# Optimization experiments

Hardware: AMD Instinct MI355X
Metric: run time of the kernel (lower is better)

The kernel has to match this reference:

```python
import jax, jax.numpy as jnp
import numpy as np

N, E, D = 50000, 800000, 64  # nodes, edges, hidden (in_hid == out_hid, n_heads == 1)


def setup_inputs() -> dict:
    key = jax.random.key(0)
    ks = jax.random.split(key, 12)

    def lin(k, out_d, in_d):
        k1, k2 = jax.random.split(k)
        s = 1.0 / np.sqrt(in_d)
        W = jax.random.uniform(k1, (out_d, in_d), minval=-s, maxval=s, dtype=jnp.float32)
        b = jax.random.uniform(k2, (out_d,), minval=-s, maxval=s, dtype=jnp.float32)
        return W, b

    Wt, bt = lin(ks[0], D, D + 1)   # w_transfer: Linear(d_input+1, d_k)
    Wq, bq = lin(ks[1], D, D)
    Wks, bks = lin(ks[2], D, D)
    Wkd, bkd = lin(ks[3], D, D)
    Wvs, bvs = lin(ks[4], D, D)
    Wvd, bvd = lin(ks[5], D, D)
    return {
        "x": jax.random.normal(ks[6], (N, D), dtype=jnp.float32),
        "edge_index": jax.random.randint(ks[7], (2, E), 0, N),
        "edge_time": jax.random.uniform(ks[8], (E,), dtype=jnp.float32),
        "x_time": jax.random.uniform(ks[9], (N,), dtype=jnp.float32),
        "edge_same": jax.random.randint(ks[10], (E,), 0, 2).astype(jnp.float32),
        "ln_gamma": jnp.ones((D,), jnp.float32),
        "ln_beta": jnp.zeros((D,), jnp.float32),
        "Wt": Wt, "bt": bt, "Wq": Wq, "bq": bq,
        "Wks": Wks, "bks": bks, "Wkd": Wkd, "bkd": bkd,
        "Wvs": Wvs, "bvs": bvs, "Wvd": Wvd, "bvd": bvd,
    }


def _gelu(x):
    return jax.nn.gelu(x, approximate=False)  # torch F.gelu default (erf)


def _temporal_enc(t):
    # TemporalEncoding: div_term[j] = 1/10000^(2*(j//2)/D); sin on even cols, cos on odd
    j = jnp.arange(D)
    div = 1.0 / jnp.power(jnp.float32(10000.0), (2.0 * (j // 2)).astype(jnp.float32) / D)
    pe = (t.reshape(-1, 1) * 200.0) * div[None, :]  # [E, D]
    return jnp.where((j % 2 == 0)[None, :], jnp.sin(pe), jnp.cos(pe))


def reference(x, edge_index, edge_time, x_time, edge_same, ln_gamma, ln_beta,
              Wt, bt, Wq, bq, Wks, bks, Wkd, bkd, Wvs, bvs, Wvd, bvd):
    residual = x
    # LayerNorm(d_input)
    mu = jnp.mean(x, axis=-1, keepdims=True)
    var = jnp.var(x, axis=-1, keepdims=True)
    xn = (x - mu) / jnp.sqrt(var + 1e-5) * ln_gamma + ln_beta

    src, dst = edge_index[0], edge_index[1]  # x_j = source, x_i = target (PyG default)
    x_j = xn[src]                            # [E, D] gather
    x_i = xn[dst]                            # [E, D] gather
    es = edge_same.reshape(-1, 1)            # [E, 1]

    te = _temporal_enc(edge_time)            # [E, D]
    xt = _gelu(jnp.concatenate([x_j, edge_time.reshape(-1, 1)], axis=1) @ Wt.T + bt) + te

    q = x_i @ Wq.T + bq
    k = es * (xt @ Wks.T + bks) + (1.0 - es) * (xt @ Wkd.T + bkd)
    att = jnp.sum(k * q, axis=-1) / jnp.sqrt(jnp.float32(D))  # [E]

    # PyG-style segment softmax over edges sharing the same receiver
    m = jax.ops.segment_max(att, dst, num_segments=N)
    m = jnp.where(jnp.isfinite(m), m, 0.0)
    ex = jnp.exp(att - m[dst])
    denom = jax.ops.segment_sum(ex, dst, num_segments=N)
    attn = ex / (denom[dst] + 1e-16)         # [E]

    v = es * (xt @ Wvs.T + bvs) + (1.0 - es) * (xt @ Wvd.T + bvd)
    aggr = jax.ops.segment_sum(attn[:, None] * v, dst, num_segments=N)  # [N, D]

    return residual + _gelu(aggr)            # dropout is identity in eval
```

## Files before the change

kernel.cpp:

```cpp
#include <hip/hip_runtime.h>
#include <hip/hip_bf16.h>
#include <math.h>

#define D 64

typedef __attribute__((ext_vector_type(8))) short bf16x8;
typedef __attribute__((ext_vector_type(8))) _Float16 f16x8;
typedef __attribute__((ext_vector_type(8))) unsigned short u16x8;
typedef __attribute__((ext_vector_type(4))) float f32x4;
typedef unsigned short u16;

__device__ __forceinline__ float gelu_erf(float x) {
    return 0.5f * x * (1.0f + erff(x * 0.70710678118654752f));
}
__device__ __forceinline__ float gelu_fast(float x) {
    float t = x * fmaf(x * x, -0.1029432f, -2.3022080f);
    float e = __builtin_amdgcn_exp2f(t);
    return x * __builtin_amdgcn_rcpf(1.0f + e);
}
__device__ __forceinline__ u16 f2bf(float v) {
    __hip_bfloat16 h = __float2bfloat16(v);
    return *(u16*)&h;
}
__device__ __forceinline__ float bf2f(u16 v) {
    return __uint_as_float(((unsigned int)v) << 16);
}
__device__ __forceinline__ u16 f2h(float v) {
    _Float16 h = (_Float16)v;
    return __builtin_bit_cast(u16, h);
}
__device__ __forceinline__ void atomic_pk_add_f16(u16* addr, float lo, float hi) {
    unsigned int p = (unsigned int)f2h(lo) | ((unsigned int)f2h(hi) << 16);
    asm volatile("global_atomic_pk_add_f16 %0, %1, off sc1" :: "v"(addr), "v"(p));
}
__device__ __forceinline__ int pi_perm(int p) { return ((p & 3) << 4) | (p >> 2); }

__device__ __forceinline__ float rowsum16(float v) {
    int x;
    x = __builtin_amdgcn_update_dpp(0, __builtin_bit_cast(int, v), 0xB1, 0xF, 0xF, true);
    v += __builtin_bit_cast(float, x);
    x = __builtin_amdgcn_update_dpp(0, __builtin_bit_cast(int, v), 0x4E, 0xF, 0xF, true);
    v += __builtin_bit_cast(float, x);
    x = __builtin_amdgcn_update_dpp(0, __builtin_bit_cast(int, v), 0x141, 0xF, 0xF, true);
    v += __builtin_bit_cast(float, x);
    x = __builtin_amdgcn_update_dpp(0, __builtin_bit_cast(int, v), 0x140, 0xF, 0xF, true);
    v += __builtin_bit_cast(float, x);
    return v;
}

__global__ __launch_bounds__(256) void prep_hist(
    const float* __restrict__ Wt, const float* __restrict__ Wq,
    const float* __restrict__ Wks, const float* __restrict__ Wkd,
    const float* __restrict__ Wvs, const float* __restrict__ Wvd,
    u16* __restrict__ WtB, u16* __restrict__ WqB,
    u16* __restrict__ WksB, u16* __restrict__ WkdB,
    u16* __restrict__ WvsB, u16* __restrict__ WvdB,
    const int* __restrict__ ei, const float* __restrict__ esame,
    int* __restrict__ cnt, int* __restrict__ rank, int E)
{
    if (blockIdx.x < 12) {
        int task = blockIdx.x * 4 + (threadIdx.x >> 6);
        int lane = threadIdx.x & 63;
        int wsel = task >> 3, f = task & 7;
        int c = lane & 15, quad = lane >> 4;
        int nt = f >> 1, kk = f & 1;
        for (int j = 0; j < 8; ++j) {
            int n = nt * 16 + c, k = kk * 32 + quad * 8 + j;
            float v; u16* dp; bool h16 = false;
            switch (wsel) {
                case 0: v = Wt[n * 65 + k];  dp = WtB;  break;
                case 1: v = Wq[n * 64 + k];  dp = WqB;  break;
                case 2: v = Wks[k * 64 + n]; dp = WksB; break;
                case 3: v = Wkd[k * 64 + n]; dp = WkdB; break;
                case 4: v = Wvs[n * 64 + pi_perm(k)]; dp = WvsB; h16 = true; break;
                default: v = Wvd[n * 64 + pi_perm(k)]; dp = WvdB; h16 = true; break;
            }
            dp[(f * 64 + lane) * 8 + j] = h16 ? f2h(v) : f2bf(v);
        }
    } else {
        int gid = (blockIdx.x - 12) * 256 + threadIdx.x;
        int stride = (gridDim.x - 12) * 256;
        int e[4]; bool v[4]; int key[4];
        #pragma unroll
        for (int j = 0; j < 4; ++j) { e[j] = gid + j * stride; v[j] = e[j] < E; }
        #pragma unroll
        for (int j = 0; j < 4; ++j) {
            if (v[j]) key[j] = 2 * ei[E + e[j]] + (esame[e[j]] > 0.5f ? 0 : 1);
        }
        int r[4];
        #pragma unroll
        for (int j = 0; j < 4; ++j) {
            if (v[j]) r[j] = atomicAdd(&cnt[key[j]], 1);
        }
        #pragma unroll
        for (int j = 0; j < 4; ++j) {
            if (v[j]) rank[e[j]] = r[j];
        }
    }
}

#define SCAN_CHUNK 2048

__global__ __launch_bounds__(256) void scan_phaseA(const int* __restrict__ cnt,
                                                   int* __restrict__ bsum, int M)
{
    int base = blockIdx.x * SCAN_CHUNK;
    int s = 0;
    for (int i = threadIdx.x; i < SCAN_CHUNK; i += 256) {
        int idx = base + i;
        s += (idx < M) ? cnt[idx] : 0;
    }
    #pragma unroll
    for (int o = 32; o; o >>= 1) s += __shfl_xor(s, o);
    __shared__ int red[4];
    if ((threadIdx.x & 63) == 0) red[threadIdx.x >> 6] = s;
    __syncthreads();
    if (threadIdx.x == 0) bsum[blockIdx.x] = red[0] + red[1] + red[2] + red[3];
}

__global__ __launch_bounds__(256) void scan_phaseC(const int* __restrict__ cnt,
                                                   const int* __restrict__ bsum,
                                                   int* __restrict__ cursor, int M)
{
    __shared__ int wsum[4];
    __shared__ int sboff;
    if (threadIdx.x < 64) {
        int v = ((int)threadIdx.x < (int)blockIdx.x) ? bsum[threadIdx.x] : 0;
        #pragma unroll
        for (int o = 32; o; o >>= 1) v += __shfl_xor(v, o);
        if (threadIdx.x == 0) sboff = v;
    }
    int base = blockIdx.x * SCAN_CHUNK;
    int i0 = base + threadIdx.x * 8;
    int vals[8];
    int tsum = 0;
    #pragma unroll
    for (int j = 0; j < 8; ++j) {
        int idx = i0 + j;
        vals[j] = (idx < M) ? cnt[idx] : 0;
        tsum += vals[j];
    }
    int lane = threadIdx.x & 63;
    int w = threadIdx.x >> 6;
    int inc = tsum;
    #pragma unroll
    for (int o = 1; o < 64; o <<= 1) {
        int v = __shfl_up(inc, o);
        if (lane >= o) inc += v;
    }
    if (lane == 63) wsum[w] = inc;
    __syncthreads();
    int woff = 0;
    #pragma unroll
    for (int k = 0; k < 4; ++k) woff += (k < w) ? wsum[k] : 0;
    int excl = woff + (inc - tsum) + sboff;
    #pragma unroll
    for (int j = 0; j < 8; ++j) {
        int idx = i0 + j;
        if (idx < M) cursor[idx] = excl;
        excl += vals[j];
    }
}

__global__ __launch_bounds__(256) void scatter_qgemm(
    const int* __restrict__ ei, const float* __restrict__ et,
    const float* __restrict__ esame, const int* __restrict__ cursor,
    const int* __restrict__ rank,
    int4* __restrict__ evk, int E, int GS,
    const float* __restrict__ x, const float* __restrict__ gamma, const float* __restrict__ beta,
    const u16* __restrict__ WqB, const u16* __restrict__ WksB, const u16* __restrict__ WkdB,
    const float* __restrict__ bq, const float* __restrict__ bks, const float* __restrict__ bkd,
    u16* __restrict__ xnb, u16* __restrict__ qk2, float* __restrict__ bq2, int N)
{
    __shared__ u16 qtile[4][16 * 64];
    __shared__ u16 stile[4][32 * 64];

    if (blockIdx.x < GS) {
        int gid = blockIdx.x * 256 + threadIdx.x;
        int stride = GS * 256;
        int e[4]; bool v[4]; int key[4]; int rk[4]; int src[4]; float tv[4];
        #pragma unroll
        for (int j = 0; j < 4; ++j) { e[j] = gid + j * stride; v[j] = e[j] < E; }
        #pragma unroll
        for (int j = 0; j < 4; ++j) {
            if (v[j]) {
                key[j] = 2 * ei[E + e[j]] + (esame[e[j]] > 0.5f ? 0 : 1);
                rk[j] = rank[e[j]];
                src[j] = ei[e[j]];
                tv[j] = et[e[j]];
            }
        }
        int pos[4];
        #pragma unroll
        for (int j = 0; j < 4; ++j) {
            if (v[j]) pos[j] = cursor[key[j]] + rk[j];
        }
        #pragma unroll
        for (int j = 0; j < 4; ++j) {
            if (v[j]) evk[pos[j]] = make_int4(key[j], __float_as_int(tv[j]), src[j], 0);
        }
        return;
    }

    const int lane = threadIdx.x & 63;
    const int c = lane & 15, quad = lane >> 4;
    const int w = threadIdx.x >> 6;
    const int wave = (blockIdx.x - GS) * 4 + w;
    const int n0r = wave * 16;
    const bool active = n0r < N;
    const int n0 = active ? n0r : 0;
    const int rowA = (n0 + c < N) ? n0 + c : N - 1;

    const float* xrow = x + (long)rowA * D;
    f32x4 xa = *(const f32x4*)(xrow + quad * 8);
    f32x4 xb = *(const f32x4*)(xrow + quad * 8 + 4);
    f32x4 xc = *(const f32x4*)(xrow + 32 + quad * 8);
    f32x4 xd = *(const f32x4*)(xrow + 32 + quad * 8 + 4);
    float s = 0.f, s2 = 0.f;
    #pragma unroll
    for (int j = 0; j < 4; ++j) {
        s += xa[j] + xb[j] + xc[j] + xd[j];
        s2 += xa[j] * xa[j] + xb[j] * xb[j] + xc[j] * xc[j] + xd[j] * xd[j];
    }
    s += __shfl_xor(s, 16);  s += __shfl_xor(s, 32);
    s2 += __shfl_xor(s2, 16); s2 += __shfl_xor(s2, 32);
    float mu = s * (1.0f / 64.0f);
    float var = s2 * (1.0f / 64.0f) - mu * mu;
    float rinv = rsqrtf(var + 1e-5f);
    f32x4 ga = *(const f32x4*)(gamma + quad * 8);
    f32x4 gb = *(const f32x4*)(gamma + quad * 8 + 4);
    f32x4 gc = *(const f32x4*)(gamma + 32 + quad * 8);
    f32x4 gd = *(const f32x4*)(gamma + 32 + quad * 8 + 4);
    f32x4 ba = *(const f32x4*)(beta + quad * 8);
    f32x4 bb = *(const f32x4*)(beta + quad * 8 + 4);
    f32x4 bc = *(const f32x4*)(beta + 32 + quad * 8);
    f32x4 bd = *(const f32x4*)(beta + 32 + quad * 8 + 4);
    bf16x8 a0, a1;
    #pragma unroll
    for (int j = 0; j < 4; ++j) {
        a0[j]     = (short)f2bf(fmaf((xa[j] - mu) * rinv, ga[j], ba[j]));
        a0[4 + j] = (short)f2bf(fmaf((xb[j] - mu) * rinv, gb[j], bb[j]));
        a1[j]     = (short)f2bf(fmaf((xc[j] - mu) * rinv, gc[j], bc[j]));
        a1[4 + j] = (short)f2bf(fmaf((xd[j] - mu) * rinv, gd[j], bd[j]));
    }
    *(bf16x8*)(xnb + (long)rowA * D + quad * 8) = a0;
    *(bf16x8*)(xnb + (long)rowA * D + 32 + quad * 8) = a1;

    float bqc[4], bksc[4], bkdc[4];
    #pragma unroll
    for (int t = 0; t < 4; ++t) {
        bqc[t] = bq[t * 16 + c]; bksc[t] = bks[t * 16 + c]; bkdc[t] = bkd[t * 16 + c];
    }

    f32x4 accq[4];
    #pragma unroll
    for (int t = 0; t < 4; ++t) {
        bf16x8 b0 = *(const bf16x8*)(WqB + ((t * 2 + 0) * 64 + lane) * 8);
        bf16x8 b1 = *(const bf16x8*)(WqB + ((t * 2 + 1) * 64 + lane) * 8);
        f32x4 z = {0.f, 0.f, 0.f, 0.f};
        z = __builtin_amdgcn_mfma_f32_16x16x32_bf16(a0, b0, z, 0, 0, 0);
        z = __builtin_amdgcn_mfma_f32_16x16x32_bf16(a1, b1, z, 0, 0, 0);
        accq[t] = z;
    }
    #pragma unroll
    for (int r = 0; r < 4; ++r) {
        float qv[4], ss = 0.f, sd = 0.f;
        #pragma unroll
        for (int t = 0; t < 4; ++t) {
            qv[t] = accq[t][r] + bqc[t];
            ss = fmaf(qv[t], bksc[t], ss);
            sd = fmaf(qv[t], bkdc[t], sd);
        }
        #pragma unroll
        for (int o = 1; o < 16; o <<= 1) { ss += __shfl_xor(ss, o); sd += __shfl_xor(sd, o); }
        int nrow = n0 + quad * 4 + r;
        if (active && c == 0 && nrow < N)
            *(float2*)(bq2 + 2 * nrow) = make_float2(ss, sd);
        #pragma unroll
        for (int t = 0; t < 4; ++t)
            qtile[w][(quad * 4 + r) * 64 + t * 16 + c] = f2bf(qv[t]);
    }
    __syncthreads();

    const u16* qrow = &qtile[w][c * 64 + quad * 8];
    bf16x8 q0 = *(const bf16x8*)(qrow);
    bf16x8 q1 = *(const bf16x8*)(qrow + 32);
    #pragma unroll
    for (int t = 0; t < 4; ++t) {
        bf16x8 bs0 = *(const bf16x8*)(WksB + ((t * 2 + 0) * 64 + lane) * 8);
        bf16x8 bs1 = *(const bf16x8*)(WksB + ((t * 2 + 1) * 64 + lane) * 8);
        bf16x8 bd0 = *(const bf16x8*)(WkdB + ((t * 2 + 0) * 64 + lane) * 8);
        bf16x8 bd1 = *(const bf16x8*)(WkdB + ((t * 2 + 1) * 64 + lane) * 8);
        f32x4 zs = {0.f, 0.f, 0.f, 0.f}, zd = {0.f, 0.f, 0.f, 0.f};
        zs = __builtin_amdgcn_mfma_f32_16x16x32_bf16(q0, bs0, zs, 0, 0, 0);
        zs = __builtin_amdgcn_mfma_f32_16x16x32_bf16(q1, bs1, zs, 0, 0, 0);
        zd = __builtin_amdgcn_mfma_f32_16x16x32_bf16(q0, bd0, zd, 0, 0, 0);
        zd = __builtin_amdgcn_mfma_f32_16x16x32_bf16(q1, bd1, zd, 0, 0, 0);
        #pragma unroll
        for (int r = 0; r < 4; ++r) {
            int m = quad * 4 + r;
            stile[w][(2 * m + 0) * 64 + c * 4 + t] = f2bf(zs[r]);
            stile[w][(2 * m + 1) * 64 + c * 4 + t] = f2bf(zd[r]);
        }
    }
    __syncthreads();
    if (active) {
        int nrows = min(16, N - n0);
        const u16x8* sp = (const u16x8*)&stile[w][0];
        u16x8* dp = (u16x8*)(qk2 + (long)(2 * n0) * D);
        int cnt8 = nrows * 16;
        for (int j = lane; j < cnt8; j += 64) dp[j] = sp[j];
    }
}

template<bool FULL>
__device__ __forceinline__ void edge_run(
    const int4* __restrict__ evk, const u16* __restrict__ xnb,
    const bf16x8* bfrag, const float* btc, const float* w64c,
    const float* dvr, float phr,
    const u16* __restrict__ qk2, const float* __restrict__ bq2,
    u16* __restrict__ A, float* __restrict__ den,
    int base, int end, int qchunk, int c, int quad)
{
    int cur_key = -1;
    float racc0 = 0.f, racc1 = 0.f, racc2 = 0.f, racc3 = 0.f, rden = 0.f;
    float qf0 = 0.f, qf1 = 0.f, qf2 = 0.f, qf3 = 0.f, bqk = 0.f;

    const int rowbase = base + (c >> 2) * qchunk + (c & 3);
    const int qbase   = base + quad * qchunk;

    for (int i = 0; i < qchunk; i += 4) {
        int eidx = rowbase + i;
        int ec = FULL ? eidx : min(eidx, end - 1);
        int srcL = ((const int*)(evk + ec))[2];

        const u16* ar = xnb + srcL * D + quad * 8;
        bf16x8 a0 = *(const bf16x8*)(ar);
        bf16x8 a1 = *(const bf16x8*)(ar + 32);

        int qb = qbase + i;
        int2 kt0 = *(const int2*)(evk + (FULL ? qb     : min(qb,     end - 1)));
        int2 kt1 = *(const int2*)(evk + (FULL ? qb + 1 : min(qb + 1, end - 1)));
        int2 kt2 = *(const int2*)(evk + (FULL ? qb + 2 : min(qb + 2, end - 1)));
        int2 kt3 = *(const int2*)(evk + (FULL ? qb + 3 : min(qb + 3, end - 1)));

        f32x4 acc[4];
        #pragma unroll
        for (int t = 0; t < 4; ++t) {
            f32x4 z = {0.f, 0.f, 0.f, 0.f};
            z = __builtin_amdgcn_mfma_f32_16x16x32_bf16(a0, bfrag[t * 2 + 0], z, 0, 0, 0);
            z = __builtin_amdgcn_mfma_f32_16x16x32_bf16(a1, bfrag[t * 2 + 1], z, 0, 0, 0);
            acc[t] = z;
        }

        #pragma unroll
        for (int r = 0; r < 4; ++r) {
            int2 kt = (r == 0) ? kt0 : (r == 1) ? kt1 : (r == 2) ? kt2 : kt3;
            int keym = kt.x;
            float tm = __int_as_float(kt.y);

            float x0 = acc[0][r] + fmaf(tm, w64c[0], btc[0]);
            float x1 = acc[1][r] + fmaf(tm, w64c[1], btc[1]);
            float x2 = acc[2][r] + fmaf(tm, w64c[2], btc[2]);
            float x3 = acc[3][r] + fmaf(tm, w64c[3], btc[3]);
            float v0 = gelu_fast(x0) + __builtin_amdgcn_sinf(fmaf(tm, dvr[0], phr));
            float v1 = gelu_fast(x1) + __builtin_amdgcn_sinf(fmaf(tm, dvr[1], phr));
            float v2 = gelu_fast(x2) + __builtin_amdgcn_sinf(fmaf(tm, dvr[2], phr));
            float v3 = gelu_fast(x3) + __builtin_amdgcn_sinf(fmaf(tm, dvr[3], phr));

            if (keym != cur_key) {
                if (cur_key >= 0) {
                    u16* ap = A + cur_key * D + c * 4;
                    atomic_pk_add_f16(ap, racc0, racc1);
                    atomic_pk_add_f16(ap + 2, racc2, racc3);
                    if (c == 0) atomicAdd(&den[cur_key], rden);
                }
                cur_key = keym;
                ushort4 q4 = *(const ushort4*)(qk2 + cur_key * D + c * 4);
                qf0 = bf2f(q4.x); qf1 = bf2f(q4.y); qf2 = bf2f(q4.z); qf3 = bf2f(q4.w);
                bqk = bq2[cur_key] * 0.18033688011f;
                racc0 = racc1 = racc2 = racc3 = 0.f;
                rden = 0.f;
            }

            float p = v0 * qf0;
            p = fmaf(v1, qf1, p);
            p = fmaf(v2, qf2, p);
            p = fmaf(v3, qf3, p);
            p = rowsum16(p);

            float ex = __builtin_amdgcn_exp2f(fmaf(p, 0.18033688011f, bqk));
            if (!FULL && (qbase + i + r >= end)) ex = 0.f;

            racc0 = fmaf(ex, v0, racc0);
            racc1 = fmaf(ex, v1, racc1);
            racc2 = fmaf(ex, v2, racc2);
            racc3 = fmaf(ex, v3, racc3);
            rden += ex;
        }
    }

    if (cur_key >= 0) {
        u16* ap = A + cur_key * D + c * 4;
        atomic_pk_add_f16(ap, racc0, racc1);
        atomic_pk_add_f16(ap + 2, racc2, racc3);
        if (c == 0) atomicAdd(&den[cur_key], rden);
    }
}

__global__ __launch_bounds__(256) void edge_pass(
    const int4* __restrict__ evk, const u16* __restrict__ xnb, const u16* __restrict__ WtB,
    const float* __restrict__ Wt, const float* __restrict__ bt,
    const u16* __restrict__ qk2, const float* __restrict__ bq2,
    u16* __restrict__ A, float* __restrict__ den, int E, int chunk)
{
    const int lane = threadIdx.x & 63;
    const int c = lane & 15, quad = lane >> 4;
    const int wave = blockIdx.x * 4 + (threadIdx.x >> 6);
    const int base = wave * chunk;
    if (base >= E) return;
    const int end = min(base + chunk, E);
    const int qchunk = chunk >> 2;

    bf16x8 bfrag[8];
    #pragma unroll
    for (int f = 0; f < 8; ++f)
        bfrag[f] = *(const bf16x8*)(WtB + (f * 64 + lane) * 8);

    float btc[4], w64c[4], dvr[4];
    #pragma unroll
    for (int t = 0; t < 4; ++t) {
        int dim = t * 16 + c;
        btc[t] = bt[dim];
        w64c[t] = Wt[dim * 65 + 64];
        dvr[t] = 31.830988618f * expf(-9.210340371976184f * (float)(2 * (dim >> 1)) * (1.0f / 64.0f));
    }
    const float phr = (c & 1) ? 0.25f : 0.0f;

    if (base + chunk <= E)
        edge_run<true>(evk, xnb, bfrag, btc, w64c, dvr, phr, qk2, bq2, A, den,
                       base, end, qchunk, c, quad);
    else
        edge_run<false>(evk, xnb, bfrag, btc, w64c, dvr, phr, qk2, bq2, A, den,
                        base, end, qchunk, c, quad);
}

__global__ __launch_bounds__(256) void vgemm(
    const float* __restrict__ x, const u16* __restrict__ A, const float* __restrict__ den,
    const u16* __restrict__ WvsB, const u16* __restrict__ WvdB,
    const float* __restrict__ bvs, const float* __restrict__ bvd,
    float* __restrict__ out, int N)
{
    const int lane = threadIdx.x & 63;
    const int c = lane & 15, quad = lane >> 4;
    const int wave = blockIdx.x * 4 + (threadIdx.x >> 6);
    const int n0 = wave * 16;
    if (n0 >= N) return;
    const int rowA = (n0 + c < N) ? n0 + c : N - 1;

    float bvsc[4], bvdc[4];
    #pragma unroll
    for (int t = 0; t < 4; ++t) { bvsc[t] = bvs[t * 16 + c]; bvdc[t] = bvd[t * 16 + c]; }

    const u16* srow = A + (long)(2 * rowA) * D + quad * 8;
    const u16* drow = A + (long)(2 * rowA + 1) * D + quad * 8;
    f16x8 s0 = *(const f16x8*)(srow);
    f16x8 s1 = *(const f16x8*)(srow + 32);
    f16x8 d0 = *(const f16x8*)(drow);
    f16x8 d1 = *(const f16x8*)(drow + 32);

    f32x4 oacc[4];
    #pragma unroll
    for (int t = 0; t < 4; ++t) {
        f16x8 bs0 = *(const f16x8*)(WvsB + ((t * 2 + 0) * 64 + lane) * 8);
        f16x8 bs1 = *(const f16x8*)(WvsB + ((t * 2 + 1) * 64 + lane) * 8);
        f16x8 bd0 = *(const f16x8*)(WvdB + ((t * 2 + 0) * 64 + lane) * 8);
        f16x8 bd1 = *(const f16x8*)(WvdB + ((t * 2 + 1) * 64 + lane) * 8);
        f32x4 z = {0.f, 0.f, 0.f, 0.f};
        z = __builtin_amdgcn_mfma_f32_16x16x32_f16(s0, bs0, z, 0, 0, 0);
        z = __builtin_amdgcn_mfma_f32_16x16x32_f16(s1, bs1, z, 0, 0, 0);
        z = __builtin_amdgcn_mfma_f32_16x16x32_f16(d0, bd0, z, 0, 0, 0);
        z = __builtin_amdgcn_mfma_f32_16x16x32_f16(d1, bd1, z, 0, 0, 0);
        oacc[t] = z;
    }

    #pragma unroll
    for (int r = 0; r < 4; ++r) {
        int n = n0 + quad * 4 + r;
        if (n >= N) continue;
        float ds = den[2 * n], dd = den[2 * n + 1];
        float inv = 1.0f / (ds + dd + 1e-16f);
        float fs = ds * inv, fd = dd * inv;
        #pragma unroll
        for (int t = 0; t < 4; ++t) {
            long idx = (long)n * D + t * 16 + c;
            float o = fmaf(oacc[t][r], inv, fmaf(fs, bvsc[t], fd * bvdc[t]));
            out[idx] = x[idx] + gelu_erf(o);
        }
    }
}

extern "C" void kernel_launch(void* const* d_in, const int* in_sizes, int n_in,
                              void* d_out, int out_size, void* d_ws, size_t ws_size,
                              hipStream_t stream) {
    const float* x        = (const float*)d_in[0];
    const int*   ei       = (const int*)d_in[1];
    const float* et       = (const float*)d_in[2];
    const float* esame    = (const float*)d_in[4];
    const float* ln_gamma = (const float*)d_in[5];
    const float* ln_beta  = (const float*)d_in[6];
    const float* Wt  = (const float*)d_in[7];
    const float* bt  = (const float*)d_in[8];
    const float* Wq  = (const float*)d_in[9];
    const float* bq  = (const float*)d_in[10];
    const float* Wks = (const float*)d_in[11];
    const float* bks = (const float*)d_in[12];
    const float* Wkd = (const float*)d_in[13];
    const float* bkd = (const float*)d_in[14];
    const float* Wvs = (const float*)d_in[15];
    const float* bvs = (const float*)d_in[16];
    const float* Wvd = (const float*)d_in[17];
    const float* bvd = (const float*)d_in[18];
    float* out = (float*)d_out;

    const int N = in_sizes[0] / D;
    const int E = in_sizes[2];
    const int M = 2 * N;

    u16* A      = (u16*)d_ws;
    float* den  = (float*)(A + (long)M * D);
    int* cnt    = (int*)(den + M);
    int* cursor = cnt + M;
    float* bq2  = (float*)(cursor + M);
    int4* evk   = (int4*)(bq2 + M);
    int* bsum   = (int*)(evk + E);
    u16* xnb    = (u16*)(bsum + 256);
    u16* qk2    = xnb + (long)N * D;
    u16* WtB    = qk2 + (long)M * D;
    u16* WqB    = WtB + 4096;
    u16* WksB   = WqB + 4096;
    u16* WkdB   = WksB + 4096;
    u16* WvsB   = WkdB + 4096;
    u16* WvdB   = WvsB + 4096;
    int* rank   = (int*)A;

    hipMemsetAsync(cnt, 0, (size_t)M * 4, stream);

    const int GH = (E + 256 * 4 - 1) / (256 * 4);
    prep_hist<<<12 + GH, 256, 0, stream>>>(Wt, Wq, Wks, Wkd, Wvs, Wvd,
                                           WtB, WqB, WksB, WkdB, WvsB, WvdB,
                                           ei, esame, cnt, rank, E);
    const int nbScan = (M + SCAN_CHUNK - 1) / SCAN_CHUNK;
    scan_phaseA<<<nbScan, 256, 0, stream>>>(cnt, bsum, M);
    scan_phaseC<<<nbScan, 256, 0, stream>>>(cnt, bsum, cursor, M);

    const int GS = (E + 256 * 4 - 1) / (256 * 4);
    const int GQ = ((N + 15) / 16 + 3) / 4;
    scatter_qgemm<<<GS + GQ, 256, 0, stream>>>(
        ei, et, esame, cursor, rank, evk, E, GS,
        x, ln_gamma, ln_beta, WqB, WksB, WkdB, bq, bks, bkd,
        xnb, qk2, bq2, N);

    hipMemsetAsync(A, 0, (size_t)M * D * 2 + (size_t)M * 4, stream);

    const int nwaves = 2048 * 4;
    const int chunk = ((E + nwaves * 16 - 1) / (nwaves * 16)) * 16;
    edge_pass<<<2048, 256, 0, stream>>>(evk, xnb, WtB, Wt, bt,
                                        qk2, bq2, A, den, E, chunk);
    vgemm<<<GQ, 256, 0, stream>>>(x, A, den, WvsB, WvdB, bvs, bvd, out, N);
}
```

Measured before the change: 233.5 us.

## Software-pipeline edge loop loads and prefetch q rows per edge

Inlines the edge loop into the kernel and adds software pipelining. The next iteration's source index, gathered xn rows and key/time records are loaded while the current MFMA and GELU work runs, and the source index is fetched two iterations ahead. Query rows and bias are now loaded for every edge up front instead of only when the destination key changes. This hides gather latency but issues more q loads and uses more registers. The FULL/partial template split is removed in favour of always clamping indices and masking.

```diff
diff --git a/kernel.cpp b/kernel.cpp
--- a/kernel.cpp
+++ b/kernel.cpp
@@ -313,101 +313,6 @@
     }
 }
 
-template<bool FULL>
-__device__ __forceinline__ void edge_run(
-    const int4* __restrict__ evk, const u16* __restrict__ xnb,
-    const bf16x8* bfrag, const float* btc, const float* w64c,
-    const float* dvr, float phr,
-    const u16* __restrict__ qk2, const float* __restrict__ bq2,
-    u16* __restrict__ A, float* __restrict__ den,
-    int base, int end, int qchunk, int c, int quad)
-{
-    int cur_key = -1;
-    float racc0 = 0.f, racc1 = 0.f, racc2 = 0.f, racc3 = 0.f, rden = 0.f;
-    float qf0 = 0.f, qf1 = 0.f, qf2 = 0.f, qf3 = 0.f, bqk = 0.f;
-
-    const int rowbase = base + (c >> 2) * qchunk + (c & 3);
-    const int qbase   = base + quad * qchunk;
-
-    for (int i = 0; i < qchunk; i += 4) {
-        int eidx = rowbase + i;
-        int ec = FULL ? eidx : min(eidx, end - 1);
-        int srcL = ((const int*)(evk + ec))[2];
-
-        const u16* ar = xnb + srcL * D + quad * 8;
-        bf16x8 a0 = *(const bf16x8*)(ar);
-        bf16x8 a1 = *(const bf16x8*)(ar + 32);
-
-        int qb = qbase + i;
-        int2 kt0 = *(const int2*)(evk + (FULL ? qb     : min(qb,     end - 1)));
-        int2 kt1 = *(const int2*)(evk + (FULL ? qb + 1 : min(qb + 1, end - 1)));
-        int2 kt2 = *(const int2*)(evk + (FULL ? qb + 2 : min(qb + 2, end - 1)));
-        int2 kt3 = *(const int2*)(evk + (FULL ? qb + 3 : min(qb + 3, end - 1)));
-
-        f32x4 acc[4];
-        #pragma unroll
-        for (int t = 0; t < 4; ++t) {
-            f32x4 z = {0.f, 0.f, 0.f, 0.f};
-            z = __builtin_amdgcn_mfma_f32_16x16x32_bf16(a0, bfrag[t * 2 + 0], z, 0, 0, 0);
-            z = __builtin_amdgcn_mfma_f32_16x16x32_bf16(a1, bfrag[t * 2 + 1], z, 0, 0, 0);
-            acc[t] = z;
-        }
-
-        #pragma unroll
-        for (int r = 0; r < 4; ++r) {
-            int2 kt = (r == 0) ? kt0 : (r == 1) ? kt1 : (r == 2) ? kt2 : kt3;
-            int keym = kt.x;
-            float tm = __int_as_float(kt.y);
-
-            float x0 = acc[0][r] + fmaf(tm, w64c[0], btc[0]);
-            float x1 = acc[1][r] + fmaf(tm, w64c[1], btc[1]);
-            float x2 = acc[2][r] + fmaf(tm, w64c[2], btc[2]);
-            float x3 = acc[3][r] + fmaf(tm, w64c[3], btc[3]);
-            float v0 = gelu_fast(x0) + __builtin_amdgcn_sinf(fmaf(tm, dvr[0], phr));
-            float v1 = gelu_fast(x1) + __builtin_amdgcn_sinf(fmaf(tm, dvr[1], phr));
-            float v2 = gelu_fast(x2) + __builtin_amdgcn_sinf(fmaf(tm, dvr[2], phr));
-            float v3 = gelu_fast(x3) + __builtin_amdgcn_sinf(fmaf(tm, dvr[3], phr));
-
-            if (keym != cur_key) {
-                if (cur_key >= 0) {
-                    u16* ap = A + cur_key * D + c * 4;
-                    atomic_pk_add_f16(ap, racc0, racc1);
-                    atomic_pk_add_f16(ap + 2, racc2, racc3);
-                    if (c == 0) atomicAdd(&den[cur_key], rden);
-                }
-                cur_key = keym;
-                ushort4 q4 = *(const ushort4*)(qk2 + cur_key * D + c * 4);
-                qf0 = bf2f(q4.x); qf1 = bf2f(q4.y); qf2 = bf2f(q4.z); qf3 = bf2f(q4.w);
-                bqk = bq2[cur_key] * 0.18033688011f;
-                racc0 = racc1 = racc2 = racc3 = 0.f;
-                rden = 0.f;
-            }
-
-            float p = v0 * qf0;
-            p = fmaf(v1, qf1, p);
-            p = fmaf(v2, qf2, p);
-            p = fmaf(v3, qf3, p);
-            p = rowsum16(p);
-
-            float ex = __builtin_amdgcn_exp2f(fmaf(p, 0.18033688011f, bqk));
-            if (!FULL && (qbase + i + r >= end)) ex = 0.f;
-
-            racc0 = fmaf(ex, v0, racc0);
-            racc1 = fmaf(ex, v1, racc1);
-            racc2 = fmaf(ex, v2, racc2);
-            racc3 = fmaf(ex, v3, racc3);
-            rden += ex;
-        }
-    }
-
-    if (cur_key >= 0) {
-        u16* ap = A + cur_key * D + c * 4;
-        atomic_pk_add_f16(ap, racc0, racc1);
-        atomic_pk_add_f16(ap + 2, racc2, racc3);
-        if (c == 0) atomicAdd(&den[cur_key], rden);
-    }
-}
-
 __global__ __launch_bounds__(256) void edge_pass(
     const int4* __restrict__ evk, const u16* __restrict__ xnb, const u16* __restrict__ WtB,
     const float* __restrict__ Wt, const float* __restrict__ bt,
@@ -420,6 +325,7 @@
     const int base = wave * chunk;
     if (base >= E) return;
     const int end = min(base + chunk, E);
+    const int last = end - 1;
     const int qchunk = chunk >> 2;
 
     bf16x8 bfrag[8];
@@ -436,13 +342,115 @@
         dvr[t] = 31.830988618f * expf(-9.210340371976184f * (float)(2 * (dim >> 1)) * (1.0f / 64.0f));
     }
     const float phr = (c & 1) ? 0.25f : 0.0f;
-
-    if (base + chunk <= E)
-        edge_run<true>(evk, xnb, bfrag, btc, w64c, dvr, phr, qk2, bq2, A, den,
-                       base, end, qchunk, c, quad);
-    else
-        edge_run<false>(evk, xnb, bfrag, btc, w64c, dvr, phr, qk2, bq2, A, den,
-                        base, end, qchunk, c, quad);
+    const float S = 0.18033688011f;
+
+    int cur_key = -1;
+    float racc0 = 0.f, racc1 = 0.f, racc2 = 0.f, racc3 = 0.f, rden = 0.f;
+
+    const int rowbase = base + (c >> 2) * qchunk + (c & 3);
+    const int qbase   = base + quad * qchunk;
+
+    {
+        int e0 = min(rowbase, last);
+        int s0 = ((const int*)(evk + e0))[2];
+        const u16* ar = xnb + s0 * D + quad * 8;
+        (void)ar;
+    }
+    int e0 = min(rowbase, last);
+    int srcC = ((const int*)(evk + e0))[2];
+    bf16x8 a0c = *(const bf16x8*)(xnb + srcC * D + quad * 8);
+    bf16x8 a1c = *(const bf16x8*)(xnb + srcC * D + quad * 8 + 32);
+    int srcN = ((const int*)(evk + min(rowbase + 4, last)))[2];
+    int2 ktc0 = *(const int2*)(evk + min(qbase,     last));
+    int2 ktc1 = *(const int2*)(evk + min(qbase + 1, last));
+    int2 ktc2 = *(const int2*)(evk + min(qbase + 2, last));
+    int2 ktc3 = *(const int2*)(evk + min(qbase + 3, last));
+
+    for (int i = 0; i < qchunk; i += 4) {
+        ushort4 q40 = *(const ushort4*)(qk2 + ktc0.x * D + c * 4);
+        ushort4 q41 = *(const ushort4*)(qk2 + ktc1.x * D + c * 4);
+        ushort4 q42 = *(const ushort4*)(qk2 + ktc2.x * D + c * 4);
+        ushort4 q43 = *(const ushort4*)(qk2 + ktc3.x * D + c * 4);
+        float bqs0 = bq2[ktc0.x] * S;
+        float bqs1 = bq2[ktc1.x] * S;
+        float bqs2 = bq2[ktc2.x] * S;
+        float bqs3 = bq2[ktc3.x] * S;
+
+        const u16* arN = xnb + srcN * D + quad * 8;
+        bf16x8 a0n = *(const bf16x8*)(arN);
+        bf16x8 a1n = *(const bf16x8*)(arN + 32);
+        int srcN2 = ((const int*)(evk + min(rowbase + i + 8, last)))[2];
+        int qn = qbase + i + 4;
+        int2 ktn0 = *(const int2*)(evk + min(qn,     last));
+        int2 ktn1 = *(const int2*)(evk + min(qn + 1, last));
+        int2 ktn2 = *(const int2*)(evk + min(qn + 2, last));
+        int2 ktn3 = *(const int2*)(evk + min(qn + 3, last));
+
+        f32x4 acc[4];
+        #pragma unroll
+        for (int t = 0; t < 4; ++t) {
+            f32x4 z = {0.f, 0.f, 0.f, 0.f};
+            z = __builtin_amdgcn_mfma_f32_16x16x32_bf16(a0c, bfrag[t * 2 + 0], z, 0, 0, 0);
+            z = __builtin_amdgcn_mfma_f32_16x16x32_bf16(a1c, bfrag[t * 2 + 1], z, 0, 0, 0);
+            acc[t] = z;
+        }
+
+        #pragma unroll
+        for (int r = 0; r < 4; ++r) {
+            int2 kt   = (r == 0) ? ktc0 : (r == 1) ? ktc1 : (r == 2) ? ktc2 : ktc3;
+            ushort4 q4 = (r == 0) ? q40 : (r == 1) ? q41 : (r == 2) ? q42 : q43;
+            float bqs  = (r == 0) ? bqs0 : (r == 1) ? bqs1 : (r == 2) ? bqs2 : bqs3;
+            int keym = kt.x;
+            float tm = __int_as_float(kt.y);
+
+            float x0 = acc[0][r] + fmaf(tm, w64c[0], btc[0]);
+            float x1 = acc[1][r] + fmaf(tm, w64c[1], btc[1]);
+            float x2 = acc[2][r] + fmaf(tm, w64c[2], btc[2]);
+            float x3 = acc[3][r] + fmaf(tm, w64c[3], btc[3]);
+            float v0 = gelu_fast(x0) + __builtin_amdgcn_sinf(fmaf(tm, dvr[0], phr));
+            float v1 = gelu_fast(x1) + __builtin_amdgcn_sinf(fmaf(tm, dvr[1], phr));
+            float v2 = gelu_fast(x2) + __builtin_amdgcn_sinf(fmaf(tm, dvr[2], phr));
+            float v3 = gelu_fast(x3) + __builtin_amdgcn_sinf(fmaf(tm, dvr[3], phr));
+
+            if (keym != cur_key) {
+                if (cur_key >= 0) {
+                    u16* ap = A + cur_key * D + c * 4;
+                    atomic_pk_add_f16(ap, racc0, racc1);
+                    atomic_pk_add_f16(ap + 2, racc2, racc3);
+                    if (c == 0) atomicAdd(&den[cur_key], rden);
+                }
+                cur_key = keym;
+                racc0 = racc1 = racc2 = racc3 = 0.f;
+                rden = 0.f;
+            }
+
+            float p = v0 * bf2f(q4.x);
+            p = fmaf(v1, bf2f(q4.y), p);
+            p = fmaf(v2, bf2f(q4.z), p);
+            p = fmaf(v3, bf2f(q4.w), p);
+            p = rowsum16(p);
+
+            float ex = __builtin_amdgcn_exp2f(fmaf(p, S, bqs));
+            ex = (qbase + i + r < end) ? ex : 0.f;
+
+            racc0 = fmaf(ex, v0, racc0);
+            racc1 = fmaf(ex, v1, racc1);
+            racc2 = fmaf(ex, v2, racc2);
+            racc3 = fmaf(ex, v3, racc3);
+            rden += ex;
+        }
+
+        srcC = srcN;  srcN = srcN2;
+        a0c = a0n;    a1c = a1n;
+        ktc0 = ktn0;  ktc1 = ktn1;  ktc2 = ktn2;  ktc3 = ktn3;
+    }
+
+    if (cur_key >= 0) {
+        u16* ap = A + cur_key * D + c * 4;
+        atomic_pk_add_f16(ap, racc0, racc1);
+        atomic_pk_add_f16(ap + 2, racc2, racc3);
+        if (c == 0) atomicAdd(&den[cur_key], rden);
+    }
 }
 
 __global__ __launch_bounds__(256) void vgemm(
```

Result: no change. 230.5 us (-1.3%).
